# Optimization experiments

Hardware: AMD Instinct MI355X
Metric: run time of the kernel (lower is better)

The kernel has to match this reference:

```python
import jax, jax.numpy as jnp
import numpy as np
from jax import lax

G = 256          # grid_size
D = 64           # state_dim
H = 128          # hidden_dim
N = 8192         # n_cells
M = 15           # force-field gaussian kernel size
SIGMA = 2.0
RADIUS2 = 25.0   # neighbor radius 5, squared
FI_T = 0.7       # fi_threshold


def _gauss1d(m, sigma, dtype):
    x = jnp.arange(m, dtype=dtype) - (m - 1) / 2.0
    k = jnp.exp(-(x * x) / (2.0 * sigma * sigma))
    return k / k.sum()


def _force_field(energy_grid, role_grid):
    # ForceField.compute_with_gradient: separable MxM gaussian smoothing of the
    # combined energy+role field, gradient via central differences.
    img = (energy_grid + 0.5 * role_grid)[None, None]  # [1,1,G,G]
    k = _gauss1d(M, SIGMA, img.dtype)
    kv = k.reshape(1, 1, M, 1)
    kh = k.reshape(1, 1, 1, M)
    f = lax.conv_general_dilated(img, kv, (1, 1), 'SAME')
    f = lax.conv_general_dilated(f, kh, (1, 1), 'SAME')[0, 0]  # [G,G]
    gy, gx = jnp.gradient(f)  # d/dy (axis 0), d/dx (axis 1)
    return f, gx, gy


def setup_inputs() -> dict:
    key = jax.random.key(0)
    ks = jax.random.split(key, 10)
    positions = jax.random.randint(ks[0], (N, 2), 0, G, dtype=jnp.int32)
    states = jax.random.normal(ks[1], (N, D), dtype=jnp.float32) * 0.1
    roles = jax.random.randint(ks[2], (N,), 0, 3, dtype=jnp.int32)
    energies = jax.random.uniform(ks[3], (N,), dtype=jnp.float32)
    s = 1.0 / np.sqrt(D)
    W_inf = jax.random.normal(ks[4], (D, D), dtype=jnp.float32) * s
    W_self = jax.random.normal(ks[5], (D, D), dtype=jnp.float32) * s
    W1 = jax.random.normal(ks[6], (D + 1, H), dtype=jnp.float32) * s
    b1 = jnp.zeros((H,), dtype=jnp.float32)
    W2 = jax.random.normal(ks[7], (H, D), dtype=jnp.float32) * (1.0 / np.sqrt(H))
    b2 = jnp.zeros((D,), dtype=jnp.float32)
    return {'positions': positions, 'states': states, 'roles': roles,
            'energies': energies, 'W_inf': W_inf, 'W_self': W_self,
            'W1': W1, 'b1': b1, 'W2': W2, 'b2': b2}


def reference(positions, states, roles, energies, W_inf, W_self, W1, b1, W2, b2):
    dt = states.dtype
    xs, ys = positions[:, 0], positions[:, 1]

    egrid = jnp.zeros((G, G), dt).at[ys, xs].max(energies)
    rgrid = jnp.zeros((G, G), dt).at[ys, xs].max(roles.astype(dt))
    field, gx, gy = _force_field(egrid, rgrid)
    potential = field[ys, xs]              # [N]
    gxc, gyc = gx[ys, xs], gy[ys, xs]

    # pairwise neighbor search (radius 5, excluding self)
    d = (positions[:, None, :] - positions[None, :, :]).astype(dt)  # [N,N,2]
    dist2 = jnp.sum(d * d, axis=-1)                                  # [N,N]
    eye = jnp.eye(N, dtype=bool)
    nbr = (dist2 <= RADIUS2) & ~eye
    mass_n = jnp.sum(nbr & (roles == 0)[None, :], axis=-1)  # int [N]
    fi_n = jnp.sum(nbr & (roles == 1)[None, :], axis=-1)
    n_nbr = jnp.sum(nbr, axis=-1)
    has = n_nbr > 0
    denom = jnp.maximum(n_nbr, 1).astype(dt)

    # bidirectional influence: pair[i,j] = tanh(s_i . W_inf . s_j)
    pair = jnp.tanh((states @ W_inf) @ states.T)          # [N,N]
    out_mean = jnp.sum(pair * nbr, axis=-1) / denom        # cell -> neighbors
    in_mean = jnp.sum(pair.T * nbr, axis=-1) / denom       # neighbors -> cell
    net = jnp.where(has, out_mean - in_mean, 0.0)

    # state update: self-similarity enrich + transform_net MLP
    self_pat = jnp.tanh(states @ W_self)
    enriched = states + 0.1 * self_pat
    v = jnp.concatenate([enriched, potential[:, None]], axis=-1)  # [N,D+1]
    transformed = jnp.tanh(v @ W1 + b1) @ W2 + b2
    new_states = jnp.where(has[:, None], transformed + 0.3 * states, states)

    # energy update
    mass_nf = mass_n.astype(dt)
    e_fi = energies + 0.02 * mass_nf
    e_other = (energies * 0.995 + 0.05 * jnp.maximum(potential, 0.0)
               + jnp.where(mass_n >= 3, 0.02, 0.0))
    new_e = jnp.where(roles == 1, e_fi, e_other) + 0.02 * jnp.maximum(net, 0.0)
    new_e = jnp.clip(new_e, 0.0, 1.0)

    # role update
    score = net + 0.5
    can_fi = (new_e > FI_T) & (mass_n >= 2) & ((fi_n == 0) | (score > 0.2))
    r0 = jnp.where(can_fi, 1, 0)
    loses = (mass_n < 1) | (new_e < 0.2) | (score < -0.3)
    r1 = jnp.where(loses, 0, 1)
    r2 = jnp.where((fi_n > 0) & (net > 0.5), 1, jnp.where(new_e < 0.2, 0, 2))
    new_roles = jnp.where(roles == 0, r0,
                          jnp.where(roles == 1, r1, r2)).astype(jnp.int32)

    # movement: mass follows gradient, corrupt chases nearest fi neighbor
    move_mass = (new_roles == 0) & ((jnp.abs(gxc) > 0.01) | (jnp.abs(gyc) > 0.01))
    dxm = jnp.sign(gxc).astype(jnp.int32)
    dym = jnp.sign(gyc).astype(jnp.int32)
    fi_mask = nbr & (roles == 1)[None, :]
    d2fi = jnp.where(fi_mask, dist2, jnp.inf)
    tgt = jnp.argmin(d2fi, axis=-1)
    dxc = jnp.sign(xs[tgt] - xs).astype(jnp.int32)
    dyc = jnp.sign(ys[tgt] - ys).astype(jnp.int32)
    move_c = (new_roles == 2) & (fi_n > 0)
    dx = jnp.where(move_mass, dxm, jnp.where(move_c, dxc, 0))
    dy = jnp.where(move_mass, dym, jnp.where(move_c, dyc, 0))
    new_pos = jnp.stack([jnp.clip(xs + dx, 0, G - 1),
                         jnp.clip(ys + dy, 0, G - 1)], axis=-1)

    return new_states, new_e, new_roles, new_pos
```

## Files before the change

kernel.cpp:

```cpp
#include <hip/hip_runtime.h>

#define N 8192
#define G 256
#define D 64
#define H 128
#define CAP 8

#define OFF_EGRID   0
#define OFF_RGRID   65536
#define OFF_FIELD   196608
#define OFF_A       262144
#define OFF_OUTSUM  1843200
#define OFF_INSUM   1851392
#define OFF_NNBR    1859584
#define OFF_MASSN   1867776
#define OFF_FIN     1875968
#define OFF_TGT     1884160
#define OFF_CELLCNT 1892352
#define OFF_BUCKET  1957888

__global__ void k_zero(float* eg, float* rg, int* cellcnt) {
    int i = blockIdx.x * blockDim.x + threadIdx.x;
    if (i < G * G) { eg[i] = 0.f; rg[i] = 0.f; cellcnt[i] = 0; }
}

__global__ void k_scatter(const int* pos, const int* roles, const float* energies,
                          float* eg, float* rg, int* cellcnt, int* bucket) {
    int i = blockIdx.x * blockDim.x + threadIdx.x;
    if (i >= N) return;
    int x = pos[2 * i], y = pos[2 * i + 1];
    int c = y * G + x;
    atomicMax((int*)&eg[c], __float_as_int(energies[i]));
    atomicMax((int*)&rg[c], __float_as_int((float)roles[i]));
    int slot = atomicAdd(&cellcnt[c], 1);
    if (slot < CAP) bucket[c * CAP + slot] = i;
}

__device__ __forceinline__ void gauss_weights(float* k) {
    float s = 0.f;
    #pragma unroll
    for (int m = 0; m < 15; m++) { float xx = (float)m - 7.f; k[m] = expf(-(xx * xx) / 8.f); s += k[m]; }
    #pragma unroll
    for (int m = 0; m < 15; m++) k[m] /= s;
}

__global__ void k_prepall(int* cellcnt, int* bucket, const float* eg, const float* rg,
                          float* field, const float* S, const float* W, float* A_) {
    __shared__ float sh[4096 + 1024];
    int t = threadIdx.x;
    if (blockIdx.x < 256) {
        int y = blockIdx.x, x = t;
        int idx = y * G + x;
        int n = cellcnt[idx]; if (n > CAP) n = CAP;
        cellcnt[idx] = n;
        for (int a = 1; a < n; a++) {
            int v = bucket[idx * CAP + a];
            int b = a - 1;
            while (b >= 0 && bucket[idx * CAP + b] > v) { bucket[idx * CAP + b + 1] = bucket[idx * CAP + b]; b--; }
            bucket[idx * CAP + b + 1] = v;
        }
        float k[15]; gauss_weights(k);
        float acc = 0.f;
        #pragma unroll
        for (int m = 0; m < 15; m++) {
            int yy = y + m - 7;
            if ((unsigned)yy < G) acc += (eg[yy * G + x] + 0.5f * rg[yy * G + x]) * k[m];
        }
        sh[x] = acc;
        __syncthreads();
        float acc2 = 0.f;
        #pragma unroll
        for (int m = 0; m < 15; m++) {
            int xx = x + m - 7;
            if ((unsigned)xx < G) acc2 += sh[xx] * k[m];
        }
        field[idx] = acc2;
    } else {
        float* Wl = sh;
        float* Sl = sh + 4096;
        const float4* W4 = (const float4*)W;
        float4* Wl4 = (float4*)Wl;
        for (int k = t; k < 1024; k += 256) Wl4[k] = W4[k];
        int row0 = (blockIdx.x - 256) * 16;
        const float4* S4 = (const float4*)(S + row0 * 64);
        float4* Sl4 = (float4*)Sl;
        for (int k = t; k < 256; k += 256) Sl4[k] = S4[k];
        __syncthreads();
        int c = t & 63, r0 = (t >> 6) * 4;
        #pragma unroll
        for (int rr = 0; rr < 4; rr++) {
            float acc = 0.f;
            #pragma unroll
            for (int k = 0; k < 64; k++) acc += Sl[(r0 + rr) * 64 + k] * Wl[k * 64 + c];
            A_[(row0 + r0 + rr) * 64 + c] = acc;
        }
    }
}

__device__ __forceinline__ float fast_tanh(float x) {
    float t = __expf(2.f * x);
    return 1.f - 2.f / (t + 1.f);
}

__device__ __forceinline__ void cell_of(int k, int& ox, int& oy, int& d2) {
    const int w[11] = {1, 7, 9, 9, 9, 11, 9, 9, 9, 7, 1};
    int acc = 0; ox = 0; oy = 0;
    #pragma unroll
    for (int r = 0; r < 11; r++) {
        bool in = (k >= acc) && (k < acc + w[r]);
        if (in) { oy = r - 5; ox = k - acc - (w[r] >> 1); }
        acc += w[r];
    }
    d2 = ox * ox + oy * oy;
}

#define NB_WAVES 4
__global__ __launch_bounds__(256) void k_neighbors(
        const int* pos, const int* roles, const float* S, const float* A_,
        const int* cellcnt, const int* bucket,
        float* outsum, float* insum, int* nnbr, int* massn, int* fin, int* tgtb) {
    __shared__ int   lds_list[NB_WAVES][656];
    __shared__ float lds_si[NB_WAVES][64];
    __shared__ float lds_ai[NB_WAVES][64];
    int wid = threadIdx.x >> 6, lane = threadIdx.x & 63;
    int i = blockIdx.x * NB_WAVES + wid;
    int xi = pos[2 * i], yi = pos[2 * i + 1];
    lds_si[wid][lane] = S[i * 64 + lane];
    lds_ai[wid][lane] = A_[i * 64 + lane];
    int cnt0 = 0, cnt1 = 0, c0 = 0, c1 = 0, d2_0 = 0, d2_1 = 0;
    {
        int ox, oy, d2; cell_of(lane, ox, oy, d2);
        int cx = xi + ox, cy = yi + oy;
        if ((unsigned)cx < G && (unsigned)cy < G) { c0 = cy * G + cx; d2_0 = d2; cnt0 = cellcnt[c0]; }
    }
    if (lane < 17) {
        int ox, oy, d2; cell_of(64 + lane, ox, oy, d2);
        int cx = xi + ox, cy = yi + oy;
        if ((unsigned)cx < G && (unsigned)cy < G) { c1 = cy * G + cx; d2_1 = d2; cnt1 = cellcnt[c1]; }
    }
    int x0 = cnt0;
    #pragma unroll
    for (int d = 1; d < 64; d <<= 1) { int y = __shfl_up(x0, d, 64); if (lane >= d) x0 += y; }
    int excl0 = x0 - cnt0, total0 = __shfl(x0, 63, 64);
    int x1 = cnt1;
    #pragma unroll
    for (int d = 1; d < 64; d <<= 1) { int y = __shfl_up(x1, d, 64); if (lane >= d) x1 += y; }
    int excl1 = x1 - cnt1, total1 = __shfl(x1, 63, 64);
    int nn_raw = total0 + total1;
    for (int s = 0; s < cnt0; s++) {
        int j = bucket[c0 * CAP + s];
        lds_list[wid][excl0 + s] = (d2_0 << 13) | j;
    }
    for (int s = 0; s < cnt1; s++) {
        int j = bucket[c1 * CAP + s];
        lds_list[wid][total0 + excl1 + s] = (d2_1 << 13) | j;
    }
    __syncthreads();
    float osum_p = 0.f, isum_p = 0.f;
    int nn = 0, mn = 0, fn = 0, bestkey = 0x7FFFFFFF;
    const float4* S4 = (const float4*)S;
    const float4* A4 = (const float4*)A_;
    const float4* si4 = (const float4*)lds_si[wid];
    const float4* ai4 = (const float4*)lds_ai[wid];
    for (int base = 0; base < nn_raw; base += 64) {
        int e = base + lane;
        bool inrange = e < nn_raw;
        int key = inrange ? lds_list[wid][e] : 0;
        int j = key & 8191;
        bool valid = inrange && (j != i);
        int rj = valid ? roles[j] : -1;
        nn += __popcll(__ballot(valid));
        mn += __popcll(__ballot(rj == 0));
        fn += __popcll(__ballot(rj == 1));
        int cand = (rj == 1) ? key : 0x7FFFFFFF;
        #pragma unroll
        for (int m = 32; m >= 1; m >>= 1) cand = min(cand, __shfl_xor(cand, m, 64));
        bestkey = min(bestkey, cand);
        if (valid) {
            const float4* srow = S4 + j * 16;
            const float4* arow = A4 + j * 16;
            float po0 = 0.f, po1 = 0.f, pi0 = 0.f, pi1 = 0.f;
            #pragma unroll
            for (int k = 0; k < 16; k += 2) {
                float4 sj = srow[k],     aj = arow[k];
                float4 av = ai4[k],      sv = si4[k];
                po0 += sj.x * av.x + sj.y * av.y + sj.z * av.z + sj.w * av.w;
                pi0 += aj.x * sv.x + aj.y * sv.y + aj.z * sv.z + aj.w * sv.w;
                float4 sj1 = srow[k + 1], aj1 = arow[k + 1];
                float4 av1 = ai4[k + 1],  sv1 = si4[k + 1];
                po1 += sj1.x * av1.x + sj1.y * av1.y + sj1.z * av1.z + sj1.w * av1.w;
                pi1 += aj1.x * sv1.x + aj1.y * sv1.y + aj1.z * sv1.z + aj1.w * sv1.w;
            }
            osum_p += fast_tanh(po0 + po1);
            isum_p += fast_tanh(pi0 + pi1);
        }
    }
    #pragma unroll
    for (int m = 32; m >= 1; m >>= 1) {
        osum_p += __shfl_xor(osum_p, m, 64);
        isum_p += __shfl_xor(isum_p, m, 64);
    }
    if (lane == 0) {
        outsum[i] = osum_p; insum[i] = isum_p;
        nnbr[i] = nn; massn[i] = mn; fin[i] = fn;
        tgtb[i] = (bestkey == 0x7FFFFFFF) ? 0 : (bestkey & 8191);
    }
}

__device__ __forceinline__ void fma4(float4& acc, float s, const float4& w) {
    acc.x += s * w.x; acc.y += s * w.y; acc.z += s * w.z; acc.w += s * w.w;
}

#define MLP_A 16
__global__ __launch_bounds__(256, 2) void k_mlp(
        const float* S, const float* Wself, const float* W1, const float* b1,
        const float* W2, const float* b2,
        const int* pos, const int* roles, const float* energies, const float* field,
        const float* outsum, const float* insum,
        const int* nnbr, const int* massn, const int* fin, const int* tgtb,
        float* out_states, float* out_e, float* out_roles, float* out_pos) {
    __shared__ float Wbuf[65 * 128];
    __shared__ float Sl[MLP_A][68];
    __shared__ float v[MLP_A][68];
    __shared__ float hl[MLP_A][132];
    int t = threadIdx.x;
    int a0 = blockIdx.x * MLP_A;
    {
        const float4* w4 = (const float4*)Wself;
        float4* dst4 = (float4*)Wbuf;
        for (int k = t; k < 1024; k += 256) dst4[k] = w4[k];
        const float4* s4 = (const float4*)(S + a0 * 64);
        {
            int a = t >> 4, q = t & 15;
            *(float4*)&Sl[a][q * 4] = s4[t];
        }
    }
    __syncthreads();
    {
        int a = t >> 4, k0 = (t & 15) * 4;
        float4 acc = {0.f, 0.f, 0.f, 0.f};
        #pragma unroll 2
        for (int kq = 0; kq < 16; kq++) {
            float4 sA = *(const float4*)&Sl[a][kq * 4];
            float4 w0 = *(const float4*)&Wbuf[(kq * 4 + 0) * 64 + k0];
            float4 w1 = *(const float4*)&Wbuf[(kq * 4 + 1) * 64 + k0];
            float4 w2 = *(const float4*)&Wbuf[(kq * 4 + 2) * 64 + k0];
            float4 w3 = *(const float4*)&Wbuf[(kq * 4 + 3) * 64 + k0];
            fma4(acc, sA.x, w0); fma4(acc, sA.y, w1); fma4(acc, sA.z, w2); fma4(acc, sA.w, w3);
        }
        float4 sv = *(const float4*)&Sl[a][k0];
        float4 o;
        o.x = sv.x + 0.1f * fast_tanh(acc.x);
        o.y = sv.y + 0.1f * fast_tanh(acc.y);
        o.z = sv.z + 0.1f * fast_tanh(acc.z);
        o.w = sv.w + 0.1f * fast_tanh(acc.w);
        *(float4*)&v[a][k0] = o;
    }
    if (t < MLP_A) {
        int ai = a0 + t;
        int x = pos[2 * ai], y = pos[2 * ai + 1];
        v[t][64] = field[y * G + x];
    }
    __syncthreads();
    {
        const float4* w4 = (const float4*)W1;
        float4* dst4 = (float4*)Wbuf;
        for (int k = t; k < 2080; k += 256) dst4[k] = w4[k];
    }
    __syncthreads();
    {
        int p = t >> 5, h0 = (t & 31) * 4;
        int aA = p, aB = p + 8;
        float4 accA = *(const float4*)&b1[h0];
        float4 accB = accA;
        #pragma unroll 2
        for (int kq = 0; kq < 16; kq++) {
            float4 vA = *(const float4*)&v[aA][kq * 4];
            float4 vB = *(const float4*)&v[aB][kq * 4];
            float4 w0 = *(const float4*)&Wbuf[(kq * 4 + 0) * 128 + h0];
            float4 w1 = *(const float4*)&Wbuf[(kq * 4 + 1) * 128 + h0];
            float4 w2 = *(const float4*)&Wbuf[(kq * 4 + 2) * 128 + h0];
            float4 w3 = *(const float4*)&Wbuf[(kq * 4 + 3) * 128 + h0];
            fma4(accA, vA.x, w0); fma4(accA, vA.y, w1); fma4(accA, vA.z, w2); fma4(accA, vA.w, w3);
            fma4(accB, vB.x, w0); fma4(accB, vB.y, w1); fma4(accB, vB.z, w2); fma4(accB, vB.w, w3);
        }
        {
            float vA64 = v[aA][64], vB64 = v[aB][64];
            float4 wt = *(const float4*)&Wbuf[64 * 128 + h0];
            fma4(accA, vA64, wt); fma4(accB, vB64, wt);
        }
        float4 oA, oB;
        oA.x = fast_tanh(accA.x); oA.y = fast_tanh(accA.y);
        oA.z = fast_tanh(accA.z); oA.w = fast_tanh(accA.w);
        oB.x = fast_tanh(accB.x); oB.y = fast_tanh(accB.y);
        oB.z = fast_tanh(accB.z); oB.w = fast_tanh(accB.w);
        *(float4*)&hl[aA][h0] = oA;
        *(float4*)&hl[aB][h0] = oB;
    }
    __syncthreads();
    {
        const float4* w4 = (const float4*)W2;
        float4* dst4 = (float4*)Wbuf;
        for (int k = t; k < 2048; k += 256) dst4[k] = w4[k];
    }
    __syncthreads();
    {
        int a = t >> 4, d0 = (t & 15) * 4;
        int i = a0 + a;
        float4 acc = *(const float4*)&b2[d0];
        #pragma unroll 2
        for (int kq = 0; kq < 32; kq++) {
            float4 hA = *(const float4*)&hl[a][kq * 4];
            float4 w0 = *(const float4*)&Wbuf[(kq * 4 + 0) * 64 + d0];
            float4 w1 = *(const float4*)&Wbuf[(kq * 4 + 1) * 64 + d0];
            float4 w2 = *(const float4*)&Wbuf[(kq * 4 + 2) * 64 + d0];
            float4 w3 = *(const float4*)&Wbuf[(kq * 4 + 3) * 64 + d0];
            fma4(acc, hA.x, w0); fma4(acc, hA.y, w1); fma4(acc, hA.z, w2); fma4(acc, hA.w, w3);
        }
        float4 sv = *(const float4*)&Sl[a][d0];
        bool has = nnbr[i] > 0;
        float4 o;
        o.x = has ? (acc.x + 0.3f * sv.x) : sv.x;
        o.y = has ? (acc.y + 0.3f * sv.y) : sv.y;
        o.z = has ? (acc.z + 0.3f * sv.z) : sv.z;
        o.w = has ? (acc.w + 0.3f * sv.w) : sv.w;
        *(float4*)&out_states[i * 64 + d0] = o;
    }
    if (t < MLP_A) {
        int i = a0 + t;
        int x = pos[2 * i], y = pos[2 * i + 1];
        float f = field[y * G + x];
        float gx = (x == 0)     ? field[y * G + 1] - field[y * G + 0]
                 : (x == G - 1) ? field[y * G + G - 1] - field[y * G + G - 2]
                                : 0.5f * (field[y * G + x + 1] - field[y * G + x - 1]);
        float gy = (y == 0)     ? field[G + x] - field[x]
                 : (y == G - 1) ? field[(G - 1) * G + x] - field[(G - 2) * G + x]
                                : 0.5f * (field[(y + 1) * G + x] - field[(y - 1) * G + x]);
        int nn = nnbr[i];
        bool has = nn > 0;
        float denom = (float)max(nn, 1);
        float net = has ? (outsum[i] / denom - insum[i] / denom) : 0.f;
        int role = roles[i];
        float e = energies[i];
        int mn = massn[i], fn = fin[i];
        float e_fi = e + 0.02f * (float)mn;
        float e_other = e * 0.995f + 0.05f * fmaxf(f, 0.f) + ((mn >= 3) ? 0.02f : 0.f);
        float new_e = ((role == 1) ? e_fi : e_other) + 0.02f * fmaxf(net, 0.f);
        new_e = fminf(fmaxf(new_e, 0.f), 1.f);
        float score = net + 0.5f;
        int r0 = ((new_e > 0.7f) && (mn >= 2) && ((fn == 0) || (score > 0.2f))) ? 1 : 0;
        int r1 = ((mn < 1) || (new_e < 0.2f) || (score < -0.3f)) ? 0 : 1;
        int r2 = ((fn > 0) && (net > 0.5f)) ? 1 : ((new_e < 0.2f) ? 0 : 2);
        int nr = (role == 0) ? r0 : (role == 1) ? r1 : r2;
        bool move_mass = (nr == 0) && ((fabsf(gx) > 0.01f) || (fabsf(gy) > 0.01f));
        int dxm = (gx > 0.f) ? 1 : ((gx < 0.f) ? -1 : 0);
        int dym = (gy > 0.f) ? 1 : ((gy < 0.f) ? -1 : 0);
        int tj = tgtb[i];
        int tx = pos[2 * tj], ty = pos[2 * tj + 1];
        int dxc = (tx > x) ? 1 : ((tx < x) ? -1 : 0);
        int dyc = (ty > y) ? 1 : ((ty < y) ? -1 : 0);
        bool move_c = (nr == 2) && (fn > 0);
        int dx = move_mass ? dxm : (move_c ? dxc : 0);
        int dy = move_mass ? dym : (move_c ? dyc : 0);
        int nx = min(max(x + dx, 0), G - 1);
        int ny = min(max(y + dy, 0), G - 1);
        out_e[i] = new_e;
        out_roles[i] = (float)nr;
        out_pos[2 * i] = (float)nx;
        out_pos[2 * i + 1] = (float)ny;
    }
}

extern "C" void kernel_launch(void* const* d_in, const int* in_sizes, int n_in,
                              void* d_out, int out_size, void* d_ws, size_t ws_size,
                              hipStream_t stream) {
    const int*   positions = (const int*)d_in[0];
    const float* states    = (const float*)d_in[1];
    const int*   roles     = (const int*)d_in[2];
    const float* energies  = (const float*)d_in[3];
    const float* W_inf     = (const float*)d_in[4];
    const float* W_self    = (const float*)d_in[5];
    const float* W1        = (const float*)d_in[6];
    const float* b1        = (const float*)d_in[7];
    const float* W2        = (const float*)d_in[8];
    const float* b2        = (const float*)d_in[9];

    float* wsf = (float*)d_ws;
    int*   wsi = (int*)d_ws;

    float* eg      = wsf + OFF_EGRID;
    float* rg      = wsf + OFF_RGRID;
    float* field   = wsf + OFF_FIELD;
    float* A_      = wsf + OFF_A;
    float* outsum  = wsf + OFF_OUTSUM;
    float* insum   = wsf + OFF_INSUM;
    int*   nnbr    = wsi + OFF_NNBR;
    int*   massn   = wsi + OFF_MASSN;
    int*   fin     = wsi + OFF_FIN;
    int*   tgtb    = wsi + OFF_TGT;
    int*   cellcnt = wsi + OFF_CELLCNT;
    int*   bucket  = wsi + OFF_BUCKET;

    float* out_states = (float*)d_out;
    float* out_e      = out_states + N * D;
    float* out_roles  = out_e + N;
    float* out_pos    = out_roles + N;

    k_zero<<<G * G / 256, 256, 0, stream>>>(eg, rg, cellcnt);
    k_scatter<<<N / 256, 256, 0, stream>>>(positions, roles, energies, eg, rg, cellcnt, bucket);
    k_prepall<<<256 + 512, 256, 0, stream>>>(cellcnt, bucket, eg, rg, field, states, W_inf, A_);
    k_neighbors<<<N / NB_WAVES, 256, 0, stream>>>(positions, roles, states, A_, cellcnt, bucket,
                                                  outsum, insum, nnbr, massn, fin, tgtb);
    k_mlp<<<N / MLP_A, 256, 0, stream>>>(states, W_self, W1, b1, W2, b2,
                                         positions, roles, energies, field, outsum, insum,
                                         nnbr, massn, fin, tgtb,
                                         out_states, out_e, out_roles, out_pos);
}
```

Measured before the change: 54.79 us.

## Replace zero+scatter kernels with per-row LDS grid/bucket build kernel

Merges the grid zeroing, global atomic scatter and the bucket sort from the prep kernel into one kernel where each block owns one grid row. Each block scans all positions, accumulates max energy, max role and bucket entries with LDS atomics for its row, sorts, then writes results. This removes two launches and the global atomics, at the cost of every block reading the full position array (256x redundant reads of 64KB, mostly cache hits).

```diff
diff --git a/kernel.cpp b/kernel.cpp
--- a/kernel.cpp
+++ b/kernel.cpp
@@ -19,23 +19,6 @@
 #define OFF_CELLCNT 1892352
 #define OFF_BUCKET  1957888
 
-__global__ void k_zero(float* eg, float* rg, int* cellcnt) {
-    int i = blockIdx.x * blockDim.x + threadIdx.x;
-    if (i < G * G) { eg[i] = 0.f; rg[i] = 0.f; cellcnt[i] = 0; }
-}
-
-__global__ void k_scatter(const int* pos, const int* roles, const float* energies,
-                          float* eg, float* rg, int* cellcnt, int* bucket) {
-    int i = blockIdx.x * blockDim.x + threadIdx.x;
-    if (i >= N) return;
-    int x = pos[2 * i], y = pos[2 * i + 1];
-    int c = y * G + x;
-    atomicMax((int*)&eg[c], __float_as_int(energies[i]));
-    atomicMax((int*)&rg[c], __float_as_int((float)roles[i]));
-    int slot = atomicAdd(&cellcnt[c], 1);
-    if (slot < CAP) bucket[c * CAP + slot] = i;
-}
-
 __device__ __forceinline__ void gauss_weights(float* k) {
     float s = 0.f;
     #pragma unroll
@@ -44,21 +27,68 @@
     for (int m = 0; m < 15; m++) k[m] /= s;
 }
 
-__global__ void k_prepall(int* cellcnt, int* bucket, const float* eg, const float* rg,
+__device__ __forceinline__ float fast_tanh(float x) {
+    float t = __expf(2.f * x);
+    return 1.f - 2.f / (t + 1.f);
+}
+
+__device__ __forceinline__ void cell_of(int k, int& ox, int& oy, int& d2) {
+    const int w[11] = {1, 7, 9, 9, 9, 11, 9, 9, 9, 7, 1};
+    int acc = 0; ox = 0; oy = 0;
+    #pragma unroll
+    for (int r = 0; r < 11; r++) {
+        bool in = (k >= acc) && (k < acc + w[r]);
+        if (in) { oy = r - 5; ox = k - acc - (w[r] >> 1); }
+        acc += w[r];
+    }
+    d2 = ox * ox + oy * oy;
+}
+
+__device__ __forceinline__ void fma4(float4& acc, float s, const float4& w) {
+    acc.x += s * w.x; acc.y += s * w.y; acc.z += s * w.z; acc.w += s * w.w;
+}
+
+__global__ __launch_bounds__(256) void k_build(const int* pos, const int* roles, const float* energies,
+                                               float* eg, float* rg, int* cellcnt, int* bucket) {
+    __shared__ int   l_cnt[256];
+    __shared__ int   l_e[256];
+    __shared__ int   l_r[256];
+    __shared__ int   l_bkt[256 * CAP];
+    int t = threadIdx.x, row = blockIdx.x;
+    l_cnt[t] = 0; l_e[t] = 0; l_r[t] = 0;
+    __syncthreads();
+    const int2* p2 = (const int2*)pos;
+    for (int a = t; a < N; a += 256) {
+        int2 xy = p2[a];
+        if (xy.y == row) {
+            int x = xy.x;
+            atomicMax(&l_e[x], __float_as_int(energies[a]));
+            atomicMax(&l_r[x], __float_as_int((float)roles[a]));
+            int slot = atomicAdd(&l_cnt[x], 1);
+            if (slot < CAP) l_bkt[x * CAP + slot] = a;
+        }
+    }
+    __syncthreads();
+    int n = l_cnt[t]; if (n > CAP) n = CAP;
+    for (int a = 1; a < n; a++) {
+        int v = l_bkt[t * CAP + a];
+        int b = a - 1;
+        while (b >= 0 && l_bkt[t * CAP + b] > v) { l_bkt[t * CAP + b + 1] = l_bkt[t * CAP + b]; b--; }
+        l_bkt[t * CAP + b + 1] = v;
+    }
+    int idx = row * G + t;
+    eg[idx] = __int_as_float(l_e[t]);
+    rg[idx] = __int_as_float(l_r[t]);
+    cellcnt[idx] = n;
+    for (int a = 0; a < n; a++) bucket[idx * CAP + a] = l_bkt[t * CAP + a];
+}
+
+__global__ void k_prepall(const float* eg, const float* rg,
                           float* field, const float* S, const float* W, float* A_) {
     __shared__ float sh[4096 + 1024];
     int t = threadIdx.x;
     if (blockIdx.x < 256) {
         int y = blockIdx.x, x = t;
-        int idx = y * G + x;
-        int n = cellcnt[idx]; if (n > CAP) n = CAP;
-        cellcnt[idx] = n;
-        for (int a = 1; a < n; a++) {
-            int v = bucket[idx * CAP + a];
-            int b = a - 1;
-            while (b >= 0 && bucket[idx * CAP + b] > v) { bucket[idx * CAP + b + 1] = bucket[idx * CAP + b]; b--; }
-            bucket[idx * CAP + b + 1] = v;
-        }
         float k[15]; gauss_weights(k);
         float acc = 0.f;
         #pragma unroll
@@ -74,7 +104,7 @@
             int xx = x + m - 7;
             if ((unsigned)xx < G) acc2 += sh[xx] * k[m];
         }
-        field[idx] = acc2;
+        field[y * G + x] = acc2;
     } else {
         float* Wl = sh;
         float* Sl = sh + 4096;
@@ -95,23 +125,6 @@
             A_[(row0 + r0 + rr) * 64 + c] = acc;
         }
     }
-}
-
-__device__ __forceinline__ float fast_tanh(float x) {
-    float t = __expf(2.f * x);
-    return 1.f - 2.f / (t + 1.f);
-}
-
-__device__ __forceinline__ void cell_of(int k, int& ox, int& oy, int& d2) {
-    const int w[11] = {1, 7, 9, 9, 9, 11, 9, 9, 9, 7, 1};
-    int acc = 0; ox = 0; oy = 0;
-    #pragma unroll
-    for (int r = 0; r < 11; r++) {
-        bool in = (k >= acc) && (k < acc + w[r]);
-        if (in) { oy = r - 5; ox = k - acc - (w[r] >> 1); }
-        acc += w[r];
-    }
-    d2 = ox * ox + oy * oy;
 }
 
 #define NB_WAVES 4
@@ -205,10 +218,6 @@
         nnbr[i] = nn; massn[i] = mn; fin[i] = fn;
         tgtb[i] = (bestkey == 0x7FFFFFFF) ? 0 : (bestkey & 8191);
     }
-}
-
-__device__ __forceinline__ void fma4(float4& acc, float s, const float4& w) {
-    acc.x += s * w.x; acc.y += s * w.y; acc.z += s * w.z; acc.w += s * w.w;
 }
 
 #define MLP_A 16
@@ -406,9 +415,8 @@
     float* out_roles  = out_e + N;
     float* out_pos    = out_roles + N;
 
-    k_zero<<<G * G / 256, 256, 0, stream>>>(eg, rg, cellcnt);
-    k_scatter<<<N / 256, 256, 0, stream>>>(positions, roles, energies, eg, rg, cellcnt, bucket);
-    k_prepall<<<256 + 512, 256, 0, stream>>>(cellcnt, bucket, eg, rg, field, states, W_inf, A_);
+    k_build<<<G, 256, 0, stream>>>(positions, roles, energies, eg, rg, cellcnt, bucket);
+    k_prepall<<<256 + 512, 256, 0, stream>>>(eg, rg, field, states, W_inf, A_);
     k_neighbors<<<N / NB_WAVES, 256, 0, stream>>>(positions, roles, states, A_, cellcnt, bucket,
                                                   outsum, insum, nnbr, massn, fin, tgtb);
     k_mlp<<<N / MLP_A, 256, 0, stream>>>(states, W_self, W1, b1, W2, b2,
```

New measurement: 56.12 us. 2.4% more time.
